# Kernel tuning notes

Hardware: AMD Instinct MI355X
Metric: run time of the kernel (lower is better)

The kernel has to match this reference:

```python
import jax, jax.numpy as jnp
import numpy as np

B, NQ = 4, 4096
HF, WF = 96, 96          # single-level feature map -> Nv = 9216
NV = HF * WF
E = 768                  # dim * num_frames = 192 * 4
NH, NP, NL = 8, 4, 1
HD = E // NH             # 96
EPS = 1e-6


def _layer_norm(x, w, b):
    m = jnp.mean(x, axis=-1, keepdims=True)
    v = jnp.var(x, axis=-1, keepdims=True)
    return (x - m) * jax.lax.rsqrt(v + EPS) * w + b


def _msda_core(value, shapes, loc, aw):
    # value: (B, Nv, H, D); loc: (B, Nq, H, L, P, 2) normalized in [0,1];
    # aw: (B, Nq, H, L, P). Bilinear sampling matching F.grid_sample
    # (align_corners=False, padding_mode='zeros'): pixel = loc * size - 0.5.
    Bn, Nv, H, D = value.shape
    Nq, P = loc.shape[1], loc.shape[4]
    out = jnp.zeros((Bn, H, Nq, D), value.dtype)
    start = 0
    for lvl in range(shapes.shape[0]):
        Hl, Wl = int(shapes[lvl, 0]), int(shapes[lvl, 1])
        v = value[:, start:start + Hl * Wl].transpose(0, 2, 1, 3)  # (B,H,S,D)
        start += Hl * Wl
        x = loc[:, :, :, lvl, :, 0] * Wl - 0.5  # (B,Nq,H,P)
        y = loc[:, :, :, lvl, :, 1] * Hl - 0.5
        x0, y0 = jnp.floor(x), jnp.floor(y)
        sampled = jnp.zeros((Bn, H, Nq, P, D), value.dtype)
        for dx in (0, 1):
            for dy in (0, 1):
                xi, yi = x0 + dx, y0 + dy
                w = (1.0 - jnp.abs(x - xi)) * (1.0 - jnp.abs(y - yi))
                valid = (xi >= 0) & (xi <= Wl - 1) & (yi >= 0) & (yi <= Hl - 1)
                idx = (jnp.clip(yi, 0, Hl - 1) * Wl
                       + jnp.clip(xi, 0, Wl - 1)).astype(jnp.int32)
                idx = idx.transpose(0, 2, 1, 3).reshape(Bn, H, Nq * P)
                g = jnp.take_along_axis(v, idx[..., None], axis=2)
                g = g.reshape(Bn, H, Nq, P, D)
                wz = jnp.where(valid, w, 0.0).transpose(0, 2, 1, 3)[..., None]
                sampled = sampled + g * wz
        awl = aw[:, :, :, lvl].transpose(0, 2, 1, 3)[..., None]  # (B,H,Nq,P,1)
        out = out + jnp.sum(sampled * awl, axis=3)
    return out.transpose(0, 2, 1, 3).reshape(Bn, Nq, H * D)


def setup_inputs():
    key = jax.random.key(0)
    ks = jax.random.split(key, 12)
    s = 0.02
    return {
        "query": jax.random.normal(ks[0], (B, NQ, E), jnp.float32),
        "reference_points": jax.random.uniform(ks[1], (B, NQ, NL, 2), jnp.float32),
        "feat": jax.random.normal(ks[2], (B, NV, E), jnp.float32),
        "spatial_shapes": jnp.array([[HF, WF]], jnp.int32),
        "level_start_index": jnp.zeros((NL,), jnp.int32),
        "ln_q_w": jnp.ones((E,), jnp.float32),
        "ln_q_b": jnp.zeros((E,), jnp.float32),
        "ln_f_w": jnp.ones((E,), jnp.float32),
        "ln_f_b": jnp.zeros((E,), jnp.float32),
        "W_value": jax.random.normal(ks[3], (E, E), jnp.float32) * s,
        "b_value": jnp.zeros((E,), jnp.float32),
        "W_off": jax.random.normal(ks[4], (E, NH * NL * NP * 2), jnp.float32) * s,
        "b_off": jax.random.normal(ks[5], (NH * NL * NP * 2,), jnp.float32) * s,
        "W_attn": jax.random.normal(ks[6], (E, NH * NL * NP), jnp.float32) * s,
        "b_attn": jnp.zeros((NH * NL * NP,), jnp.float32),
        "W_out": jax.random.normal(ks[7], (E, E), jnp.float32) * s,
        "b_out": jnp.zeros((E,), jnp.float32),
        "gamma": jax.random.normal(ks[8], (E,), jnp.float32) * s,
    }


def reference(query, reference_points, feat, spatial_shapes, level_start_index,
              ln_q_w, ln_q_b, ln_f_w, ln_f_b, W_value, b_value, W_off, b_off,
              W_attn, b_attn, W_out, b_out, gamma):
    shapes = np.asarray(spatial_shapes)  # static level shapes
    Bn, Nq, _ = query.shape
    Nv = feat.shape[1]
    q = _layer_norm(query, ln_q_w, ln_q_b)
    f = _layer_norm(feat, ln_f_w, ln_f_b)
    value = (f @ W_value + b_value).reshape(Bn, Nv, NH, HD)
    offsets = (q @ W_off + b_off).reshape(Bn, Nq, NH, NL, NP, 2)
    aw = jax.nn.softmax((q @ W_attn + b_attn).reshape(Bn, Nq, NH, NL * NP), -1)
    aw = aw.reshape(Bn, Nq, NH, NL, NP)
    # offset_normalizer = [W_l, H_l] per level
    norm = jnp.stack([jnp.asarray(shapes[:, 1], jnp.float32),
                      jnp.asarray(shapes[:, 0], jnp.float32)], axis=-1)  # (L,2)
    loc = (reference_points[:, :, None, :, None, :]
           + offsets / norm[None, None, None, :, None, :])
    out = _msda_core(value, shapes, loc, aw)
    out = out @ W_out + b_out
    attn = q + out  # mmcv MSDeformAttn adds identity (dropout=eval no-op)
    return query + gamma * attn
```

## Files before the change

### kernel.cpp

```cpp
#include <hip/hip_runtime.h>

#define BB     4
#define NQS    4096
#define NVS    9216
#define E_DIM  768
#define NHEAD  8
#define NPTS   4
#define HDIM   96
#define HFEAT  96
#define WFEAT  96

typedef __attribute__((ext_vector_type(8))) short  s8v;
typedef __attribute__((ext_vector_type(4))) short  s4v;
typedef __attribute__((ext_vector_type(4))) float  f4v;

__device__ __forceinline__ unsigned short f2bf(float x) {
    unsigned int u = __builtin_bit_cast(unsigned int, x);
    unsigned int r = (u + 0x7fffu + ((u >> 16) & 1u)) >> 16;
    return (unsigned short)r;
}
__device__ __forceinline__ float bf2f(unsigned short s) {
    unsigned int u = ((unsigned int)s) << 16;
    return __builtin_bit_cast(float, u);
}
__device__ __forceinline__ float bf2f_s(short s) {
    return bf2f((unsigned short)s);
}

#define GLD16(gp, lp) \
    __builtin_amdgcn_global_load_lds( \
        (__attribute__((address_space(1))) void*)(gp), \
        (__attribute__((address_space(3))) void*)(lp), 16, 0, 0)

template <bool STATS>
__global__ __launch_bounds__(192) void ln_cast_kernel(
    const float* __restrict__ x, const float* __restrict__ w,
    const float* __restrict__ b, unsigned short* __restrict__ out,
    float* __restrict__ stats) {
    const int row = blockIdx.x;
    const int t = threadIdx.x;
    const float4 v = ((const float4*)(x + (size_t)row * E_DIM))[t];
    float s1 = v.x + v.y + v.z + v.w;
    float s2 = v.x * v.x + v.y * v.y + v.z * v.z + v.w * v.w;

    __shared__ float sh[8];
    #pragma unroll
    for (int o = 32; o > 0; o >>= 1) {
        s1 += __shfl_down(s1, o, 64);
        s2 += __shfl_down(s2, o, 64);
    }
    const int lane = t & 63, wv = t >> 6;
    if (lane == 0) { sh[wv * 2] = s1; sh[wv * 2 + 1] = s2; }
    __syncthreads();
    if (t == 0) {
        float a = sh[0] + sh[2] + sh[4];
        float c = sh[1] + sh[3] + sh[5];
        float mean = a * (1.0f / E_DIM);
        float var = c * (1.0f / E_DIM) - mean * mean;
        sh[6] = mean;
        sh[7] = rsqrtf(var + 1e-6f);
        if (STATS) { stats[row * 2 + 0] = sh[6]; stats[row * 2 + 1] = sh[7]; }
    }
    __syncthreads();
    const float mean = sh[6], rstd = sh[7];
    const float4 w4 = ((const float4*)w)[t];
    const float4 b4 = ((const float4*)b)[t];
    s4v o;
    o[0] = (short)f2bf((v.x - mean) * rstd * w4.x + b4.x);
    o[1] = (short)f2bf((v.y - mean) * rstd * w4.y + b4.y);
    o[2] = (short)f2bf((v.z - mean) * rstd * w4.z + b4.z);
    o[3] = (short)f2bf((v.w - mean) * rstd * w4.w + b4.w);
    ((s4v*)(out + (size_t)row * E_DIM))[t] = o;
}

__global__ void transpose_cast_kernel(const float* __restrict__ W, unsigned short* __restrict__ Wt) {
    __shared__ float tile[32][33];
    const int bi = blockIdx.y * 32, bj = blockIdx.x * 32;
    const int t = threadIdx.x;
    const int r = t >> 5, c = t & 31;
    #pragma unroll
    for (int i = 0; i < 4; i++)
        tile[r + i * 8][c] = W[(size_t)(bi + r + i * 8) * E_DIM + bj + c];
    __syncthreads();
    #pragma unroll
    for (int i = 0; i < 4; i++)
        Wt[(size_t)(bj + r + i * 8) * E_DIM + bi + c] = f2bf(tile[c][r + i * 8]);
}

__global__ void build_wqc_kernel(const float* __restrict__ W_off, const float* __restrict__ W_attn,
                                 const float* __restrict__ b_off, const float* __restrict__ b_attn,
                                 unsigned short* __restrict__ Wt, float* __restrict__ bcat) {
    const int idx = blockIdx.x * 256 + threadIdx.x;
    const int rrow = idx / E_DIM, k = idx % E_DIM;
    float v = 0.f;
    if (rrow < 64) v = W_off[(size_t)k * 64 + rrow];
    else if (rrow < 96) v = W_attn[(size_t)k * 32 + (rrow - 64)];
    Wt[idx] = f2bf(v);
    if (idx < 128) {
        float b = 0.f;
        if (idx < 64) b = b_off[idx];
        else if (idx < 96) b = b_attn[idx - 64];
        bcat[idx] = b;
    }
}

template <int EPI>
__global__ __launch_bounds__(256, 3) void mfma_gemm(
    const unsigned short* __restrict__ A, const unsigned short* __restrict__ Bt,
    const float* __restrict__ bias, void* __restrict__ C, int ldC,
    const float* __restrict__ query, const float* __restrict__ qstats,
    const float* __restrict__ lnw, const float* __restrict__ lnb,
    const float* __restrict__ gamma) {
    __shared__ unsigned short As[128 * 64];
    __shared__ unsigned short Bs[128 * 64];

    constexpr int K = E_DIM;
    const int tid = threadIdx.x;
    const int wave = tid >> 6;
    const int lane = tid & 63;
    const int quad = lane >> 4;
    const int l16 = lane & 15;

    const int nwg = gridDim.x * gridDim.y;
    const int flat = blockIdx.y * gridDim.x + blockIdx.x;
    const int cpx = nwg >> 3;
    const int swz = (flat & 7) * cpx + (flat >> 3);
    const int bx = swz % gridDim.x;
    const int by = swz / gridDim.x;
    const int bm = by * 128;
    const int bn = bx * 128;
    const int wrow = wave >> 1, wcol = wave & 1;

    const unsigned short* arow[4];
    const unsigned short* brow[4];
    unsigned short* aldst[4];
    unsigned short* bldst[4];
    #pragma unroll
    for (int i = 0; i < 4; i++) {
        const int chunk = wave * 4 + i;
        const int s = chunk >> 1, r = (chunk & 1) * 64 + lane;
        arow[i] = A + (size_t)(bm + r) * K + s * 8;
        brow[i] = Bt + (size_t)(bn + r) * K + s * 8;
        aldst[i] = As + chunk * 512;
        bldst[i] = Bs + chunk * 512;
    }

    f4v acc[4][4] = {};

    for (int k0 = 0; k0 < K; k0 += 64) {
        #pragma unroll
        for (int i = 0; i < 4; i++)
            GLD16(arow[i] + k0, aldst[i]);
        #pragma unroll
        for (int i = 0; i < 4; i++)
            GLD16(brow[i] + k0, bldst[i]);

        __syncthreads();

        #pragma unroll
        for (int c = 0; c < 2; c++) {
            s8v af[4], bf[4];
            #pragma unroll
            for (int ti = 0; ti < 4; ti++)
                af[ti] = *(const s8v*)(As + ((size_t)((c * 4 + quad) * 128 + wrow * 64 + ti * 16 + l16)) * 8);
            #pragma unroll
            for (int tj = 0; tj < 4; tj++)
                bf[tj] = *(const s8v*)(Bs + ((size_t)((c * 4 + quad) * 128 + wcol * 64 + tj * 16 + l16)) * 8);
            #pragma unroll
            for (int ti = 0; ti < 4; ti++)
                #pragma unroll
                for (int tj = 0; tj < 4; tj++)
                    acc[ti][tj] = __builtin_amdgcn_mfma_f32_16x16x32_bf16(af[ti], bf[tj], acc[ti][tj], 0, 0, 0);
        }
        __syncthreads();
    }

    #pragma unroll
    for (int ti = 0; ti < 4; ti++) {
        const int gm_base = bm + wrow * 64 + ti * 16 + quad * 4;
        #pragma unroll
        for (int tj = 0; tj < 4; tj++) {
            const int gn = bn + wcol * 64 + tj * 16 + l16;
            const float bv = bias[gn];
            #pragma unroll
            for (int r = 0; r < 4; r++) {
                const int gm = gm_base + r;
                const float v = acc[ti][tj][r] + bv;
                if (EPI == 0) {
                    const int b = gm / NVS, s = gm - b * NVS;
                    const int hh = gn / HDIM, dd = gn - hh * HDIM;
                    const size_t vidx = (((size_t)b * NHEAD + hh) * NVS + s) * HDIM + dd;
                    ((unsigned short*)C)[vidx] = f2bf(v);
                } else if (EPI == 1) {
                    ((float*)C)[(size_t)gm * ldC + gn] = v;
                } else {
                    const size_t idx = (size_t)gm * ldC + gn;
                    const float qv = query[idx];
                    const float qln = (qv - qstats[gm * 2]) * qstats[gm * 2 + 1] * lnw[gn] + lnb[gn];
                    ((float*)C)[idx] = qv + gamma[gn] * (qln + v);
                }
            }
        }
    }
}

__global__ __launch_bounds__(384) void msda_kernel(
    const unsigned short* __restrict__ value,
    const float* __restrict__ oa,
    const float* __restrict__ refp,
    unsigned short* __restrict__ out) {
    const int h = blockIdx.x;
    const int row0 = blockIdx.y * 32;
    const int t = threadIdx.x;

    __shared__ float x_s[128], y_s[128], aw_s[128];
    if (t < 32) {
        const int row = row0 + t;
        const float* oar = oa + (size_t)row * 128;
        float a0 = oar[64 + h * 4 + 0], a1 = oar[64 + h * 4 + 1];
        float a2 = oar[64 + h * 4 + 2], a3 = oar[64 + h * 4 + 3];
        float mx = fmaxf(fmaxf(a0, a1), fmaxf(a2, a3));
        float e0 = __expf(a0 - mx), e1 = __expf(a1 - mx);
        float e2 = __expf(a2 - mx), e3 = __expf(a3 - mx);
        float inv = 1.0f / (e0 + e1 + e2 + e3);
        float rx = refp[(size_t)row * 2 + 0] * WFEAT - 0.5f;
        float ry = refp[(size_t)row * 2 + 1] * HFEAT - 0.5f;
        aw_s[t * 4 + 0] = e0 * inv;
        aw_s[t * 4 + 1] = e1 * inv;
        aw_s[t * 4 + 2] = e2 * inv;
        aw_s[t * 4 + 3] = e3 * inv;
        #pragma unroll
        for (int p = 0; p < 4; p++) {
            x_s[t * 4 + p] = rx + oar[h * 8 + p * 2 + 0];
            y_s[t * 4 + p] = ry + oar[h * 8 + p * 2 + 1];
        }
    }
    __syncthreads();

    const int r = t / 12;
    const int j = t - r * 12;
    const int row = row0 + r;
    const int b = row >> 12;
    const unsigned short* vb = value + ((size_t)(b * NHEAD + h) * NVS) * HDIM + j * 8;

    float acc[8] = {};
    #pragma unroll
    for (int p = 0; p < 4; p++) {
        const float x = x_s[r * 4 + p];
        const float y = y_s[r * 4 + p];
        const float aw = aw_s[r * 4 + p];
        const float x0f = floorf(x), y0f = floorf(y);
        const float fx = x - x0f, fy = y - y0f;
        const int ix0 = (int)x0f, iy0 = (int)y0f;
        const int ix1 = ix0 + 1, iy1 = iy0 + 1;
        const float wx0 = (ix0 >= 0 && ix0 < WFEAT) ? (1.f - fx) : 0.f;
        const float wx1 = (ix1 >= 0 && ix1 < WFEAT) ? fx : 0.f;
        const float wy0 = (iy0 >= 0 && iy0 < HFEAT) ? (1.f - fy) : 0.f;
        const float wy1 = (iy1 >= 0 && iy1 < HFEAT) ? fy : 0.f;
        const int cx0 = min(max(ix0, 0), WFEAT - 1);
        const int cx1 = min(max(ix1, 0), WFEAT - 1);
        const int cy0 = min(max(iy0, 0), HFEAT - 1);
        const int cy1 = min(max(iy1, 0), HFEAT - 1);
        const float w00 = aw * wy0 * wx0, w01 = aw * wy0 * wx1;
        const float w10 = aw * wy1 * wx0, w11 = aw * wy1 * wx1;
        const s8v v00 = *(const s8v*)(vb + (size_t)(cy0 * WFEAT + cx0) * HDIM);
        const s8v v01 = *(const s8v*)(vb + (size_t)(cy0 * WFEAT + cx1) * HDIM);
        const s8v v10 = *(const s8v*)(vb + (size_t)(cy1 * WFEAT + cx0) * HDIM);
        const s8v v11 = *(const s8v*)(vb + (size_t)(cy1 * WFEAT + cx1) * HDIM);
        #pragma unroll
        for (int k = 0; k < 8; k++) {
            acc[k] += w00 * bf2f_s(v00[k]) + w01 * bf2f_s(v01[k])
                    + w10 * bf2f_s(v10[k]) + w11 * bf2f_s(v11[k]);
        }
    }

    s8v o;
    #pragma unroll
    for (int k = 0; k < 8; k++) o[k] = (short)f2bf(acc[k]);
    *(s8v*)(out + (size_t)row * E_DIM + h * HDIM + j * 8) = o;
}

extern "C" void kernel_launch(void* const* d_in, const int* in_sizes, int n_in,
                              void* d_out, int out_size, void* d_ws, size_t ws_size,
                              hipStream_t stream) {
    (void)in_sizes; (void)n_in; (void)out_size; (void)ws_size;

    const float* query  = (const float*)d_in[0];
    const float* refp   = (const float*)d_in[1];
    const float* feat   = (const float*)d_in[2];
    const float* ln_q_w = (const float*)d_in[5];
    const float* ln_q_b = (const float*)d_in[6];
    const float* ln_f_w = (const float*)d_in[7];
    const float* ln_f_b = (const float*)d_in[8];
    const float* W_val  = (const float*)d_in[9];
    const float* b_val  = (const float*)d_in[10];
    const float* W_off  = (const float*)d_in[11];
    const float* b_off  = (const float*)d_in[12];
    const float* W_attn = (const float*)d_in[13];
    const float* b_attn = (const float*)d_in[14];
    const float* W_out  = (const float*)d_in[15];
    const float* b_out  = (const float*)d_in[16];
    const float* gamma  = (const float*)d_in[17];
    float* out = (float*)d_out;

    const int MQ = BB * NQS;
    const int MV = BB * NVS;

    char* ws = (char*)d_ws;
    float*          q_stats = (float*)(ws + 0);
    unsigned short* qbf     = (unsigned short*)(ws + 131072);
    unsigned short* fbf     = (unsigned short*)(ws + 25296896);
    unsigned short* val_bf  = (unsigned short*)(ws + 81920000);
    unsigned short* msda_bf = (unsigned short*)(ws + 138543104);
    float*          offattn = (float*)(ws + 163708928);
    unsigned short* Wv_t    = (unsigned short*)(ws + 172097536);
    unsigned short* Wo_t    = (unsigned short*)(ws + 173277184);
    unsigned short* Wqc_t   = (unsigned short*)(ws + 174456832);
    float*          bcat    = (float*)(ws + 174653440);

    ln_cast_kernel<true><<<MQ, 192, 0, stream>>>(query, ln_q_w, ln_q_b, qbf, q_stats);
    ln_cast_kernel<false><<<MV, 192, 0, stream>>>(feat, ln_f_w, ln_f_b, fbf, nullptr);

    transpose_cast_kernel<<<dim3(24, 24), 256, 0, stream>>>(W_val, Wv_t);
    transpose_cast_kernel<<<dim3(24, 24), 256, 0, stream>>>(W_out, Wo_t);
    build_wqc_kernel<<<384, 256, 0, stream>>>(W_off, W_attn, b_off, b_attn, Wqc_t, bcat);

    mfma_gemm<0><<<dim3(E_DIM / 128, MV / 128), 256, 0, stream>>>(
        fbf, Wv_t, b_val, val_bf, E_DIM, nullptr, nullptr, nullptr, nullptr, nullptr);

    mfma_gemm<1><<<dim3(1, MQ / 128), 256, 0, stream>>>(
        qbf, Wqc_t, bcat, offattn, 128, nullptr, nullptr, nullptr, nullptr, nullptr);

    msda_kernel<<<dim3(NHEAD, MQ / 32), 384, 0, stream>>>(val_bf, offattn, refp, msda_bf);

    mfma_gemm<2><<<dim3(E_DIM / 128, MQ / 128), 256, 0, stream>>>(
        msda_bf, Wo_t, b_out, out, E_DIM, query, q_stats, ln_q_w, ln_q_b, gamma);
}
```

Before: 482.0 us.

## Double-buffer LDS tiles in MFMA GEMM to overlap loads with compute

Splits the shared-memory A/B tiles into two buffers and prefetches the next K-slice via direct global-to-LDS loads while MFMAs consume the current one, with a peeled final iteration. This removes one barrier per K step and hides global load latency behind matrix math. It doubles LDS use to 64 KB per block and lowers the launch-bounds occupancy hint from 3 to 2 blocks per CU.

```diff
diff --git a/kernel.cpp b/kernel.cpp
--- a/kernel.cpp
+++ b/kernel.cpp
@@ -105,16 +105,17 @@
 }
 
 template <int EPI>
-__global__ __launch_bounds__(256, 3) void mfma_gemm(
+__global__ __launch_bounds__(256, 2) void mfma_gemm(
     const unsigned short* __restrict__ A, const unsigned short* __restrict__ Bt,
     const float* __restrict__ bias, void* __restrict__ C, int ldC,
     const float* __restrict__ query, const float* __restrict__ qstats,
     const float* __restrict__ lnw, const float* __restrict__ lnb,
     const float* __restrict__ gamma) {
-    __shared__ unsigned short As[128 * 64];
-    __shared__ unsigned short Bs[128 * 64];
+    __shared__ unsigned short As[2][128 * 64];
+    __shared__ unsigned short Bs[2][128 * 64];
 
     constexpr int K = E_DIM;
+    constexpr int NT = K / 64;
     const int tid = threadIdx.x;
     const int wave = tid >> 6;
     const int lane = tid & 63;
@@ -133,39 +134,43 @@
 
     const unsigned short* arow[4];
     const unsigned short* brow[4];
-    unsigned short* aldst[4];
-    unsigned short* bldst[4];
+    int ldsoff[4];
     #pragma unroll
     for (int i = 0; i < 4; i++) {
         const int chunk = wave * 4 + i;
         const int s = chunk >> 1, r = (chunk & 1) * 64 + lane;
         arow[i] = A + (size_t)(bm + r) * K + s * 8;
         brow[i] = Bt + (size_t)(bn + r) * K + s * 8;
-        aldst[i] = As + chunk * 512;
-        bldst[i] = Bs + chunk * 512;
+        ldsoff[i] = chunk * 512;
     }
 
     f4v acc[4][4] = {};
 
-    for (int k0 = 0; k0 < K; k0 += 64) {
-        #pragma unroll
-        for (int i = 0; i < 4; i++)
-            GLD16(arow[i] + k0, aldst[i]);
-        #pragma unroll
-        for (int i = 0; i < 4; i++)
-            GLD16(brow[i] + k0, bldst[i]);
-
-        __syncthreads();
-
+    #pragma unroll
+    for (int i = 0; i < 4; i++) GLD16(arow[i], &As[0][ldsoff[i]]);
+    #pragma unroll
+    for (int i = 0; i < 4; i++) GLD16(brow[i], &Bs[0][ldsoff[i]]);
+    __syncthreads();
+
+    int cur = 0;
+    for (int t = 0; t < NT - 1; ++t) {
+        const int knext = (t + 1) * 64;
+        #pragma unroll
+        for (int i = 0; i < 4; i++) GLD16(arow[i] + knext, &As[cur ^ 1][ldsoff[i]]);
+        #pragma unroll
+        for (int i = 0; i < 4; i++) GLD16(brow[i] + knext, &Bs[cur ^ 1][ldsoff[i]]);
+
+        const unsigned short* as = As[cur];
+        const unsigned short* bs = Bs[cur];
         #pragma unroll
         for (int c = 0; c < 2; c++) {
             s8v af[4], bf[4];
             #pragma unroll
             for (int ti = 0; ti < 4; ti++)
-                af[ti] = *(const s8v*)(As + ((size_t)((c * 4 + quad) * 128 + wrow * 64 + ti * 16 + l16)) * 8);
+                af[ti] = *(const s8v*)(as + ((size_t)((c * 4 + quad) * 128 + wrow * 64 + ti * 16 + l16)) * 8);
             #pragma unroll
             for (int tj = 0; tj < 4; tj++)
-                bf[tj] = *(const s8v*)(Bs + ((size_t)((c * 4 + quad) * 128 + wcol * 64 + tj * 16 + l16)) * 8);
+                bf[tj] = *(const s8v*)(bs + ((size_t)((c * 4 + quad) * 128 + wcol * 64 + tj * 16 + l16)) * 8);
             #pragma unroll
             for (int ti = 0; ti < 4; ti++)
                 #pragma unroll
@@ -173,6 +178,27 @@
                     acc[ti][tj] = __builtin_amdgcn_mfma_f32_16x16x32_bf16(af[ti], bf[tj], acc[ti][tj], 0, 0, 0);
         }
         __syncthreads();
+        cur ^= 1;
+    }
+
+    {
+        const unsigned short* as = As[cur];
+        const unsigned short* bs = Bs[cur];
+        #pragma unroll
+        for (int c = 0; c < 2; c++) {
+            s8v af[4], bf[4];
+            #pragma unroll
+            for (int ti = 0; ti < 4; ti++)
+                af[ti] = *(const s8v*)(as + ((size_t)((c * 4 + quad) * 128 + wrow * 64 + ti * 16 + l16)) * 8);
+            #pragma unroll
+            for (int tj = 0; tj < 4; tj++)
+                bf[tj] = *(const s8v*)(bs + ((size_t)((c * 4 + quad) * 128 + wcol * 64 + tj * 16 + l16)) * 8);
+            #pragma unroll
+            for (int ti = 0; ti < 4; ti++)
+                #pragma unroll
+                for (int tj = 0; tj < 4; tj++)
+                    acc[ti][tj] = __builtin_amdgcn_mfma_f32_16x16x32_bf16(af[ti], bf[tj], acc[ti][tj], 0, 0, 0);
+        }
     }
 
     #pragma unroll
```

Result: slower. 536.3 us (+11.3%).

## Load GEMM MFMA fragments directly from global memory instead of LDS staging

Applied to the files above, without the earlier changes.

The bf16 MFMA GEMM no longer stages 128x64 A/B tiles in shared memory through global_load_lds with barriers. Each wave now reads its 16-row fragments straight from global memory per k-step of 32, with the loop fully unrolled, and the occupancy hint rises from 3 to 4 blocks. This removes the LDS traffic and __syncthreads, but each A and B row is now fetched by two waves instead of once per block, so the kernel depends on L1/L2 to absorb the duplicate reads. The 16-byte strided accesses per lane are also less coalesced than the tile copies.

```diff
diff --git a/kernel.cpp b/kernel.cpp
--- a/kernel.cpp
+++ b/kernel.cpp
@@ -26,11 +26,6 @@
 __device__ __forceinline__ float bf2f_s(short s) {
     return bf2f((unsigned short)s);
 }
-
-#define GLD16(gp, lp) \
-    __builtin_amdgcn_global_load_lds( \
-        (__attribute__((address_space(1))) void*)(gp), \
-        (__attribute__((address_space(3))) void*)(lp), 16, 0, 0)
 
 template <bool STATS>
 __global__ __launch_bounds__(192) void ln_cast_kernel(
@@ -105,15 +100,12 @@
 }
 
 template <int EPI>
-__global__ __launch_bounds__(256, 3) void mfma_gemm(
+__global__ __launch_bounds__(256, 4) void mfma_gemm(
     const unsigned short* __restrict__ A, const unsigned short* __restrict__ Bt,
     const float* __restrict__ bias, void* __restrict__ C, int ldC,
     const float* __restrict__ query, const float* __restrict__ qstats,
     const float* __restrict__ lnw, const float* __restrict__ lnb,
     const float* __restrict__ gamma) {
-    __shared__ unsigned short As[128 * 64];
-    __shared__ unsigned short Bs[128 * 64];
-
     constexpr int K = E_DIM;
     const int tid = threadIdx.x;
     const int wave = tid >> 6;
@@ -131,48 +123,31 @@
     const int bn = bx * 128;
     const int wrow = wave >> 1, wcol = wave & 1;
 
-    const unsigned short* arow[4];
-    const unsigned short* brow[4];
-    unsigned short* aldst[4];
-    unsigned short* bldst[4];
-    #pragma unroll
-    for (int i = 0; i < 4; i++) {
-        const int chunk = wave * 4 + i;
-        const int s = chunk >> 1, r = (chunk & 1) * 64 + lane;
-        arow[i] = A + (size_t)(bm + r) * K + s * 8;
-        brow[i] = Bt + (size_t)(bn + r) * K + s * 8;
-        aldst[i] = As + chunk * 512;
-        bldst[i] = Bs + chunk * 512;
-    }
+    const unsigned short* abase[4];
+    const unsigned short* bbase[4];
+    #pragma unroll
+    for (int ti = 0; ti < 4; ti++)
+        abase[ti] = A + (size_t)(bm + wrow * 64 + ti * 16 + l16) * K + quad * 8;
+    #pragma unroll
+    for (int tj = 0; tj < 4; tj++)
+        bbase[tj] = Bt + (size_t)(bn + wcol * 64 + tj * 16 + l16) * K + quad * 8;
 
     f4v acc[4][4] = {};
 
-    for (int k0 = 0; k0 < K; k0 += 64) {
-        #pragma unroll
-        for (int i = 0; i < 4; i++)
-            GLD16(arow[i] + k0, aldst[i]);
-        #pragma unroll
-        for (int i = 0; i < 4; i++)
-            GLD16(brow[i] + k0, bldst[i]);
-
-        __syncthreads();
-
-        #pragma unroll
-        for (int c = 0; c < 2; c++) {
-            s8v af[4], bf[4];
-            #pragma unroll
-            for (int ti = 0; ti < 4; ti++)
-                af[ti] = *(const s8v*)(As + ((size_t)((c * 4 + quad) * 128 + wrow * 64 + ti * 16 + l16)) * 8);
+    #pragma unroll
+    for (int k = 0; k < K; k += 32) {
+        s8v af[4], bf[4];
+        #pragma unroll
+        for (int ti = 0; ti < 4; ti++)
+            af[ti] = *(const s8v*)(abase[ti] + k);
+        #pragma unroll
+        for (int tj = 0; tj < 4; tj++)
+            bf[tj] = *(const s8v*)(bbase[tj] + k);
+        #pragma unroll
+        for (int ti = 0; ti < 4; ti++)
             #pragma unroll
             for (int tj = 0; tj < 4; tj++)
-                bf[tj] = *(const s8v*)(Bs + ((size_t)((c * 4 + quad) * 128 + wcol * 64 + tj * 16 + l16)) * 8);
-            #pragma unroll
-            for (int ti = 0; ti < 4; ti++)
-                #pragma unroll
-                for (int tj = 0; tj < 4; tj++)
-                    acc[ti][tj] = __builtin_amdgcn_mfma_f32_16x16x32_bf16(af[ti], bf[tj], acc[ti][tj], 0, 0, 0);
-        }
-        __syncthreads();
+                acc[ti][tj] = __builtin_amdgcn_mfma_f32_16x16x32_bf16(af[ti], bf[tj], acc[ti][tj], 0, 0, 0);
     }
 
     #pragma unroll
```

Result: slower. 602.3 us (+25.0%).

## Add double-buffered 256x256 MFMA GEMM with interleaved prefetch for value/output projections

Applied to the files above, without the earlier changes.

Adds a new 512-thread GEMM kernel with 256x256 tiles and double-buffered LDS. The next K-tile's global loads are split into four chunks, each issued between quarter-phases of MFMA work, and those MFMA phases run at raised wave priority. The value projection and output projection GEMMs now use this kernel, while the small offset/attention GEMM stays on the old 128-tile kernel. The goal is to hide global-to-LDS latency and raise data reuse per tile. In exchange, the output projection grid shrinks to 192 workgroups, LDS use per block grows, and occupancy drops.

```diff
diff --git a/kernel.cpp b/kernel.cpp
--- a/kernel.cpp
+++ b/kernel.cpp
@@ -105,7 +105,7 @@
 }
 
 template <int EPI>
-__global__ __launch_bounds__(256, 3) void mfma_gemm(
+__global__ __launch_bounds__(256, 3) void mfma_gemm128(
     const unsigned short* __restrict__ A, const unsigned short* __restrict__ Bt,
     const float* __restrict__ bias, void* __restrict__ C, int ldC,
     const float* __restrict__ query, const float* __restrict__ qstats,
@@ -178,6 +178,172 @@
     #pragma unroll
     for (int ti = 0; ti < 4; ti++) {
         const int gm_base = bm + wrow * 64 + ti * 16 + quad * 4;
+        #pragma unroll
+        for (int tj = 0; tj < 4; tj++) {
+            const int gn = bn + wcol * 64 + tj * 16 + l16;
+            const float bv = bias[gn];
+            #pragma unroll
+            for (int r = 0; r < 4; r++) {
+                const int gm = gm_base + r;
+                const float v = acc[ti][tj][r] + bv;
+                if (EPI == 0) {
+                    const int b = gm / NVS, s = gm - b * NVS;
+                    const int hh = gn / HDIM, dd = gn - hh * HDIM;
+                    const size_t vidx = (((size_t)b * NHEAD + hh) * NVS + s) * HDIM + dd;
+                    ((unsigned short*)C)[vidx] = f2bf(v);
+                } else if (EPI == 1) {
+                    ((float*)C)[(size_t)gm * ldC + gn] = v;
+                } else {
+                    const size_t idx = (size_t)gm * ldC + gn;
+                    const float qv = query[idx];
+                    const float qln = (qv - qstats[gm * 2]) * qstats[gm * 2 + 1] * lnw[gn] + lnb[gn];
+                    ((float*)C)[idx] = qv + gamma[gn] * (qln + v);
+                }
+            }
+        }
+    }
+}
+
+template <int QQ>
+__device__ __forceinline__ void qphase(const unsigned short* as_, const unsigned short* bs_,
+                                       f4v (&acc)[8][4], int quad, int l16, int wrow, int wcol) {
+    #pragma unroll
+    for (int c = 0; c < 2; c++) {
+        s8v af[4], bf[2];
+        #pragma unroll
+        for (int m = 0; m < 4; m++)
+            af[m] = *(const s8v*)(as_ + ((size_t)((c * 4 + quad) * 256 + wrow * 128 + ((QQ >> 1) * 4 + m) * 16 + l16)) * 8);
+        #pragma unroll
+        for (int n = 0; n < 2; n++)
+            bf[n] = *(const s8v*)(bs_ + ((size_t)((c * 4 + quad) * 256 + wcol * 64 + ((QQ & 1) * 2 + n) * 16 + l16)) * 8);
+        #pragma unroll
+        for (int m = 0; m < 4; m++)
+            #pragma unroll
+            for (int n = 0; n < 2; n++)
+                acc[(QQ >> 1) * 4 + m][(QQ & 1) * 2 + n] =
+                    __builtin_amdgcn_mfma_f32_16x16x32_bf16(af[m], bf[n],
+                        acc[(QQ >> 1) * 4 + m][(QQ & 1) * 2 + n], 0, 0, 0);
+    }
+}
+
+template <int EPI>
+__global__ __launch_bounds__(512, 2) void mfma_gemm256(
+    const unsigned short* __restrict__ A, const unsigned short* __restrict__ Bt,
+    const float* __restrict__ bias, void* __restrict__ C, int ldC,
+    const float* __restrict__ query, const float* __restrict__ qstats,
+    const float* __restrict__ lnw, const float* __restrict__ lnb,
+    const float* __restrict__ gamma) {
+    __shared__ unsigned short As[2][256 * 64];
+    __shared__ unsigned short Bs[2][256 * 64];
+
+    constexpr int K = E_DIM;
+    constexpr int NT = K / 64;
+    const int tid = threadIdx.x;
+    const int wave = tid >> 6;
+    const int lane = tid & 63;
+    const int quad = lane >> 4;
+    const int l16 = lane & 15;
+
+    const int nwg = gridDim.x * gridDim.y;
+    const int flat = blockIdx.y * gridDim.x + blockIdx.x;
+    const int cpx = nwg >> 3;
+    const int swz = (flat & 7) * cpx + (flat >> 3);
+    const int bx = swz % gridDim.x;
+    const int by = swz / gridDim.x;
+    const int bm = by * 256;
+    const int bn = bx * 256;
+    const int wrow = wave >> 2;
+    const int wcol = wave & 3;
+
+    const unsigned short* gsrc[4][2];
+    int ldst[4][2];
+    #pragma unroll
+    for (int h = 0; h < 4; h++) {
+        #pragma unroll
+        for (int i = 0; i < 2; i++) {
+            const int ch = wave * 2 + i;
+            const int s = ch >> 1, rsub = ch & 1;
+            const int rw = (h & 1) * 128 + rsub * 64 + lane;
+            const unsigned short* base = (h < 2) ? (A + (size_t)(bm + rw) * K)
+                                                 : (Bt + (size_t)(bn + rw) * K);
+            gsrc[h][i] = base + s * 8;
+            ldst[h][i] = (s * 256 + rw) * 8;
+        }
+    }
+
+    #define STAGE256(h, kt, buf) do { \
+        unsigned short* lb_ = ((h) < 2 ? &As[(buf)][0] : &Bs[(buf)][0]); \
+        GLD16(gsrc[h][0] + (size_t)(kt) * 64, lb_ + ldst[h][0]); \
+        GLD16(gsrc[h][1] + (size_t)(kt) * 64, lb_ + ldst[h][1]); \
+    } while (0)
+
+    f4v acc[8][4] = {};
+
+    #pragma unroll
+    for (int h = 0; h < 4; h++) STAGE256(h, 0, 0);
+
+    int cur = 0;
+    for (int t = 0; t < NT; ++t) {
+        const unsigned short* as_ = &As[cur][0];
+        const unsigned short* bs_ = &Bs[cur][0];
+        const int nb = cur ^ 1;
+        const bool pf = (t + 1 < NT);
+
+        if (pf) {
+            STAGE256(0, t + 1, nb);
+            asm volatile("s_waitcnt vmcnt(2)" ::: "memory");
+        } else {
+            asm volatile("s_waitcnt vmcnt(0)" ::: "memory");
+        }
+        __builtin_amdgcn_s_barrier();
+        __builtin_amdgcn_sched_barrier(0);
+        __builtin_amdgcn_s_setprio(1);
+        qphase<0>(as_, bs_, acc, quad, l16, wrow, wcol);
+        __builtin_amdgcn_s_setprio(0);
+
+        if (pf) STAGE256(1, t + 1, nb);
+        __builtin_amdgcn_s_setprio(1);
+        qphase<1>(as_, bs_, acc, quad, l16, wrow, wcol);
+        __builtin_amdgcn_s_setprio(0);
+
+        if (pf) STAGE256(2, t + 1, nb);
+        __builtin_amdgcn_s_setprio(1);
+        qphase<2>(as_, bs_, acc, quad, l16, wrow, wcol);
+        __builtin_amdgcn_s_setprio(0);
+
+        if (pf) STAGE256(3, t + 1, nb);
+        s8v af3[2][4], bf3[2][2];
+        #pragma unroll
+        for (int c = 0; c < 2; c++) {
+            #pragma unroll
+            for (int m = 0; m < 4; m++)
+                af3[c][m] = *(const s8v*)(as_ + ((size_t)((c * 4 + quad) * 256 + wrow * 128 + (4 + m) * 16 + l16)) * 8);
+            #pragma unroll
+            for (int n = 0; n < 2; n++)
+                bf3[c][n] = *(const s8v*)(bs_ + ((size_t)((c * 4 + quad) * 256 + wcol * 64 + (2 + n) * 16 + l16)) * 8);
+        }
+        asm volatile("s_waitcnt lgkmcnt(0)" ::: "memory");
+        __builtin_amdgcn_sched_barrier(0);
+        __builtin_amdgcn_s_barrier();
+        __builtin_amdgcn_sched_barrier(0);
+        __builtin_amdgcn_s_setprio(1);
+        #pragma unroll
+        for (int c = 0; c < 2; c++)
+            #pragma unroll
+            for (int m = 0; m < 4; m++)
+                #pragma unroll
+                for (int n = 0; n < 2; n++)
+                    acc[4 + m][2 + n] = __builtin_amdgcn_mfma_f32_16x16x32_bf16(
+                        af3[c][m], bf3[c][n], acc[4 + m][2 + n], 0, 0, 0);
+        __builtin_amdgcn_s_setprio(0);
+
+        cur ^= 1;
+    }
+    #undef STAGE256
+
+    #pragma unroll
+    for (int ti = 0; ti < 8; ti++) {
+        const int gm_base = bm + wrow * 128 + ti * 16 + quad * 4;
         #pragma unroll
         for (int tj = 0; tj < 4; tj++) {
             const int gn = bn + wcol * 64 + tj * 16 + l16;
@@ -325,14 +491,14 @@
     transpose_cast_kernel<<<dim3(24, 24), 256, 0, stream>>>(W_out, Wo_t);
     build_wqc_kernel<<<384, 256, 0, stream>>>(W_off, W_attn, b_off, b_attn, Wqc_t, bcat);
 
-    mfma_gemm<0><<<dim3(E_DIM / 128, MV / 128), 256, 0, stream>>>(
+    mfma_gemm256<0><<<dim3(E_DIM / 256, MV / 256), 512, 0, stream>>>(
         fbf, Wv_t, b_val, val_bf, E_DIM, nullptr, nullptr, nullptr, nullptr, nullptr);
 
-    mfma_gemm<1><<<dim3(1, MQ / 128), 256, 0, stream>>>(
+    mfma_gemm128<1><<<dim3(1, MQ / 128), 256, 0, stream>>>(
         qbf, Wqc_t, bcat, offattn, 128, nullptr, nullptr, nullptr, nullptr, nullptr);
 
     msda_kernel<<<dim3(NHEAD, MQ / 32), 384, 0, stream>>>(val_bf, offattn, refp, msda_bf);
 
-    mfma_gemm<2><<<dim3(E_DIM / 128, MQ / 128), 256, 0, stream>>>(
+    mfma_gemm256<2><<<dim3(E_DIM / 256, MQ / 256), 512, 0, stream>>>(
         msda_bf, Wo_t, b_out, out, E_DIM, query, q_stats, ln_q_w, ln_q_b, gamma);
 }
```

Result: no change. 476.0 us (-1.2%).
